# Optimization experiments

Hardware: AMD Instinct MI355X
Metric: run time of the kernel (lower is better)

The kernel has to match this reference:

```python
import jax, jax.numpy as jnp
import numpy as np

DIM = 1024
EXPANSION = 4
NUM_EXPERTS = 8
N_TOKENS = 4096
CAPACITY_FACTOR = 1.0  # also becomes the gate's k -> top-1 (bug-faithful)
EPS = 1e-6


def setup_inputs() -> dict:
    key = jax.random.key(0)
    ks = jax.random.split(key, 7)
    h = DIM * EXPANSION
    s = 0.02
    return {
        "x": jax.random.normal(ks[0], (N_TOKENS, DIM), dtype=jnp.float32),
        "w_gate": jax.random.normal(ks[1], (DIM, NUM_EXPERTS), dtype=jnp.float32) * s,
        "b_gate": jnp.zeros((NUM_EXPERTS,), dtype=jnp.float32),
        "w1": jax.random.normal(ks[2], (NUM_EXPERTS, DIM, h), dtype=jnp.float32) * s,
        "b1": jnp.zeros((NUM_EXPERTS, h), dtype=jnp.float32),
        "w2": jax.random.normal(ks[3], (NUM_EXPERTS, h, DIM), dtype=jnp.float32) * s,
        "b2": jnp.zeros((NUM_EXPERTS, DIM), dtype=jnp.float32),
    }


def fast_gelu(x):
    return x * jax.nn.sigmoid(1.702 * x)


def switch_gate(x, w_gate, b_gate):
    # x: [n, d] -> gate_scores: [n, e]
    gate_scores = jax.nn.softmax(x @ w_gate + b_gate, axis=-1)
    capacity = int(CAPACITY_FACTOR * x.shape[0])
    k = int(CAPACITY_FACTOR)  # SwitchMoE passes capacity_factor as k -> top-1
    _, top_k_idx = jax.lax.top_k(gate_scores, k)  # [n, k]
    mask = jnp.zeros_like(gate_scores).at[
        jnp.arange(x.shape[0])[:, None], top_k_idx
    ].set(1.0)
    masked = gate_scores * mask
    denom = masked.sum(axis=0, keepdims=True) + EPS  # [1, e]
    gate_scores = masked / denom * capacity
    # aux loss (use_aux_loss=True in SwitchMoE)
    load = gate_scores.sum(axis=0)               # [e]
    importance = gate_scores.sum(axis=1).mean()  # scalar
    loss = jnp.mean((load - importance) ** 2)
    return gate_scores, loss


def reference(x, w_gate, b_gate, w1, b1, w2, b2):
    gate_scores, loss = switch_gate(x, w_gate, b_gate)  # [n, e], scalar
    # dense compute-all-experts (faithful to the naive module)
    h = fast_gelu(jnp.einsum("nd,edh->enh", x, w1) + b1[:, None, :])  # [e, n, h]
    expert_out = jnp.einsum("enh,ehd->end", h, w2) + b2[:, None, :]   # [e, n, d]
    # weighted combine: sum_e gate[n,e] * expert_out[e,n,d]
    moe_output = jnp.einsum("ne,end->nd", gate_scores, expert_out)
    return moe_output, loss
```

## Files before the change

kernel.cpp:

```cpp
#include <hip/hip_runtime.h>
#include <hip/hip_bf16.h>
#include <math.h>

#define DIMK   1024
#define HDIM   4096
#define NEXP   8
#define NTOK   4096
#define EPSV   1e-6f

typedef __attribute__((ext_vector_type(4))) float  f32x4;
typedef __attribute__((ext_vector_type(8))) __bf16 bf16x8;
typedef __attribute__((ext_vector_type(4))) __bf16 bf16x4;
typedef __attribute__((ext_vector_type(2))) __bf16 bf16x2;

__device__ __forceinline__ __bf16 f2bf(float f) { return (__bf16)f; }

__global__ void init_kernel(int* counts, int* cursors, float* S) {
    int t = threadIdx.x;
    if (t < NEXP) { counts[t] = 0; cursors[t] = 0; S[t] = 0.0f; }
}

__global__ __launch_bounds__(256) void gate_kernel(
    const float* __restrict__ x, const float* __restrict__ wg,
    const float* __restrict__ bg,
    float* S, int* counts, float* score_top, int* texp)
{
    int n = blockIdx.x;
    int t = threadIdx.x;
    f32x4 xv = *(const f32x4*)(x + (size_t)n * DIMK + t * 4);

    float p[NEXP];
#pragma unroll
    for (int e = 0; e < NEXP; e++) p[e] = 0.0f;
#pragma unroll
    for (int j = 0; j < 4; j++) {
        int d = t * 4 + j;
        f32x4 wa = *(const f32x4*)(wg + (size_t)d * NEXP);
        f32x4 wb = *(const f32x4*)(wg + (size_t)d * NEXP + 4);
#pragma unroll
        for (int e = 0; e < 4; e++) { p[e] += xv[j] * wa[e]; p[e + 4] += xv[j] * wb[e]; }
    }
#pragma unroll
    for (int e = 0; e < NEXP; e++) {
#pragma unroll
        for (int off = 32; off > 0; off >>= 1)
            p[e] += __shfl_down(p[e], off, 64);
    }
    __shared__ float red[4][NEXP];
    int lane = t & 63, wv = t >> 6;
    if (lane == 0) {
#pragma unroll
        for (int e = 0; e < NEXP; e++) red[wv][e] = p[e];
    }
    __syncthreads();
    if (t == 0) {
        float l[NEXP]; float m = -1e30f;
#pragma unroll
        for (int e = 0; e < NEXP; e++) {
            l[e] = red[0][e] + red[1][e] + red[2][e] + red[3][e] + bg[e];
            m = fmaxf(m, l[e]);
        }
        float pe[NEXP]; float s = 0.0f;
#pragma unroll
        for (int e = 0; e < NEXP; e++) { pe[e] = __expf(l[e] - m); s += pe[e]; }
        int best = 0; float bv = pe[0];
#pragma unroll
        for (int e = 1; e < NEXP; e++) if (pe[e] > bv) { bv = pe[e]; best = e; }
        float sc = bv / s;
        score_top[n] = sc;
        texp[n] = best;
        atomicAdd(&S[best], sc);
        atomicAdd(&counts[best], 1);
    }
}

__global__ void finalize_kernel(const float* S, const int* counts,
                                int* offsets, float* loss_out)
{
    if (threadIdx.x == 0 && blockIdx.x == 0) {
        int off = 0;
        float loadv[NEXP]; float tot = 0.0f;
        for (int e = 0; e < NEXP; e++) { offsets[e] = off; off += counts[e]; }
        for (int e = 0; e < NEXP; e++) {
            loadv[e] = S[e] / (S[e] + EPSV) * (float)NTOK;
            tot += loadv[e];
        }
        float imp = tot / (float)NTOK;
        float loss = 0.0f;
        for (int e = 0; e < NEXP; e++) { float d = loadv[e] - imp; loss += d * d; }
        loss_out[0] = loss / (float)NEXP;
    }
}

__global__ __launch_bounds__(256) void assign_kernel(
    const int* __restrict__ texp, const float* __restrict__ score_top,
    const float* __restrict__ S, const int* __restrict__ offsets,
    int* cursors, int* perm, float* gatew)
{
    int n = blockIdx.x * 256 + threadIdx.x;
    int e = texp[n];
    int pos = atomicAdd(&cursors[e], 1);
    perm[offsets[e] + pos] = n;
    gatew[n] = score_top[n] / (S[e] + EPSV) * (float)NTOK;
}

__global__ __launch_bounds__(256) void bias_init_kernel(
    const int* __restrict__ texp, const float* __restrict__ gatew,
    const float* __restrict__ b2, float* __restrict__ out)
{
    int n = blockIdx.x;
    int t = threadIdx.x;
    int e = texp[n];
    float g = gatew[n];
    f32x4 b = *(const f32x4*)(b2 + (size_t)e * DIMK + t * 4);
    f32x4 o = { b.x * g, b.y * g, b.z * g, b.w * g };
    *(f32x4*)(out + (size_t)n * DIMK + t * 4) = o;
}

__global__ __launch_bounds__(256) void gemm1_kernel(
    const float* __restrict__ x, const float* __restrict__ w1,
    const float* __restrict__ b1,
    const int* __restrict__ perm, const int* __restrict__ counts,
    const int* __restrict__ offsets, __bf16* __restrict__ hbuf)
{
    int bx  = blockIdx.x;
    int e   = bx >> 10;
    int rem = bx & 1023;
    int mt  = rem >> 5;
    int nt  = rem & 31;
    int ce  = counts[e];
    int m0  = mt * 128;
    if (m0 >= ce) return;
    int off = offsets[e];
    int n0  = nt * 128;
    const float* B = w1 + (size_t)e * DIMK * HDIM;

    __shared__ __bf16 As[128][40];
    __shared__ __bf16 Bs[128][40];

    int t = threadIdx.x;

    const float* aptr[4];
#pragma unroll
    for (int i = 0; i < 4; i++) {
        int r  = (t >> 3) + 32 * i;
        int ri = (m0 + r < ce) ? (m0 + r) : (ce - 1);
        aptr[i] = x + (size_t)perm[off + ri] * DIMK;
    }
    int ac4 = (t & 7) * 4;

    int n4 = ((t >> 3) & 31) * 4;
    int kp = t & 7;
    const float* Bb = B + n0 + n4;

    int lane = t & 63;
    int wv   = t >> 6;
    int wm   = (wv >> 1) * 64;
    int wn   = (wv & 1) * 64;
    int lr   = lane & 15;
    int lq   = lane >> 4;

    f32x4 acc[4][4];
#pragma unroll
    for (int mi = 0; mi < 4; mi++)
#pragma unroll
        for (int ni = 0; ni < 4; ni++) acc[mi][ni] = (f32x4)0.0f;

    for (int k0 = 0; k0 < DIMK; k0 += 32) {
#pragma unroll
        for (int i = 0; i < 4; i++) {
            int r = (t >> 3) + 32 * i;
            f32x4 v = *(const f32x4*)(aptr[i] + k0 + ac4);
            bf16x4 s4 = { f2bf(v.x), f2bf(v.y), f2bf(v.z), f2bf(v.w) };
            *(bf16x4*)&As[r][ac4] = s4;
        }
#pragma unroll
        for (int i = 0; i < 2; i++) {
            int p = kp + 8 * i;
            const float* p0 = Bb + (size_t)(k0 + 2 * p) * HDIM;
            f32x4 v0 = *(const f32x4*)p0;
            f32x4 v1 = *(const f32x4*)(p0 + HDIM);
#pragma unroll
            for (int j = 0; j < 4; j++) {
                bf16x2 w = { f2bf(v0[j]), f2bf(v1[j]) };
                *(bf16x2*)&Bs[n4 + j][2 * p] = w;
            }
        }
        __syncthreads();

        bf16x8 af[4], bfr[4];
#pragma unroll
        for (int i = 0; i < 4; i++) {
            af[i]  = *(const bf16x8*)&As[wm + i * 16 + lr][lq * 8];
            bfr[i] = *(const bf16x8*)&Bs[wn + i * 16 + lr][lq * 8];
        }
#pragma unroll
        for (int mi = 0; mi < 4; mi++)
#pragma unroll
            for (int ni = 0; ni < 4; ni++)
                acc[mi][ni] = __builtin_amdgcn_mfma_f32_16x16x32_bf16(
                    af[mi], bfr[ni], acc[mi][ni], 0, 0, 0);
        __syncthreads();
    }

    const float* b1e = b1 + (size_t)e * HDIM;
#pragma unroll
    for (int mi = 0; mi < 4; mi++) {
#pragma unroll
        for (int r = 0; r < 4; r++) {
            int i = m0 + wm + mi * 16 + lq * 4 + r;
            if (i < ce) {
                __bf16* hrow = hbuf + (size_t)(off + i) * HDIM;
#pragma unroll
                for (int ni = 0; ni < 4; ni++) {
                    int j = n0 + wn + ni * 16 + lr;
                    float v = acc[mi][ni][r] + b1e[j];
                    v = v / (1.0f + __expf(-1.702f * v));
                    hrow[j] = f2bf(v);
                }
            }
        }
    }
}

__global__ __launch_bounds__(256) void gemm2_kernel(
    const __bf16* __restrict__ hbuf, const float* __restrict__ w2,
    const int* __restrict__ perm, const int* __restrict__ counts,
    const int* __restrict__ offsets, const float* __restrict__ gatew,
    float* __restrict__ out)
{
    int bx  = blockIdx.x;
    int sk  = bx & 1;
    int rest = bx >> 1;
    int e   = rest >> 9;
    int rem = rest & 511;
    int mt  = rem >> 3;
    int nt  = rem & 7;
    int ce  = counts[e];
    int m0  = mt * 64;
    if (m0 >= ce) return;
    int off = offsets[e];
    int n0  = nt * 128;
    const float* B = w2 + (size_t)e * HDIM * DIMK;

    __shared__ __bf16 As[64][72];
    __shared__ __bf16 Bs[128][72];

    int t = threadIdx.x;

    const __bf16* aptr[2];
#pragma unroll
    for (int i = 0; i < 2; i++) {
        int r  = (t >> 3) + 32 * i;
        int ri = (m0 + r < ce) ? (m0 + r) : (ce - 1);
        aptr[i] = hbuf + (size_t)(off + ri) * HDIM;
    }
    int ac8 = (t & 7) * 8;

    int n4 = ((t >> 3) & 31) * 4;
    int kp = t & 7;
    const float* Bb = B + n0 + n4;

    int lane = t & 63;
    int wv   = t >> 6;
    int wm   = (wv >> 1) * 32;
    int wn   = (wv & 1) * 64;
    int lr   = lane & 15;
    int lq   = lane >> 4;

    f32x4 acc[2][4];
#pragma unroll
    for (int mi = 0; mi < 2; mi++)
#pragma unroll
        for (int ni = 0; ni < 4; ni++) acc[mi][ni] = (f32x4)0.0f;

    int kbeg = sk * (HDIM / 2);
    int kend = kbeg + HDIM / 2;
    for (int k0 = kbeg; k0 < kend; k0 += 64) {
#pragma unroll
        for (int i = 0; i < 2; i++) {
            int r = (t >> 3) + 32 * i;
            bf16x8 v = *(const bf16x8*)(aptr[i] + k0 + ac8);
            *(bf16x8*)&As[r][ac8] = v;
        }
#pragma unroll
        for (int i = 0; i < 4; i++) {
            int p = kp + 8 * i;
            const float* p0 = Bb + (size_t)(k0 + 2 * p) * DIMK;
            f32x4 v0 = *(const f32x4*)p0;
            f32x4 v1 = *(const f32x4*)(p0 + DIMK);
#pragma unroll
            for (int j = 0; j < 4; j++) {
                bf16x2 w = { f2bf(v0[j]), f2bf(v1[j]) };
                *(bf16x2*)&Bs[n4 + j][2 * p] = w;
            }
        }
        __syncthreads();

#pragma unroll
        for (int ks = 0; ks < 2; ks++) {
            bf16x8 af[2], bfr[4];
#pragma unroll
            for (int i = 0; i < 2; i++)
                af[i] = *(const bf16x8*)&As[wm + i * 16 + lr][lq * 8 + ks * 32];
#pragma unroll
            for (int i = 0; i < 4; i++)
                bfr[i] = *(const bf16x8*)&Bs[wn + i * 16 + lr][lq * 8 + ks * 32];
#pragma unroll
            for (int mi = 0; mi < 2; mi++)
#pragma unroll
                for (int ni = 0; ni < 4; ni++)
                    acc[mi][ni] = __builtin_amdgcn_mfma_f32_16x16x32_bf16(
                        af[mi], bfr[ni], acc[mi][ni], 0, 0, 0);
        }
        __syncthreads();
    }

#pragma unroll
    for (int mi = 0; mi < 2; mi++) {
#pragma unroll
        for (int r = 0; r < 4; r++) {
            int i = m0 + wm + mi * 16 + lq * 4 + r;
            if (i < ce) {
                int tok = perm[off + i];
                float g = gatew[tok];
                float* orow = out + (size_t)tok * DIMK;
#pragma unroll
                for (int ni = 0; ni < 4; ni++) {
                    int j = n0 + wn + ni * 16 + lr;
                    atomicAdd(&orow[j], acc[mi][ni][r] * g);
                }
            }
        }
    }
}

extern "C" void kernel_launch(void* const* d_in, const int* in_sizes, int n_in,
                              void* d_out, int out_size, void* d_ws, size_t ws_size,
                              hipStream_t stream)
{
    const float* x  = (const float*)d_in[0];
    const float* wg = (const float*)d_in[1];
    const float* bg = (const float*)d_in[2];
    const float* w1 = (const float*)d_in[3];
    const float* b1 = (const float*)d_in[4];
    const float* w2 = (const float*)d_in[5];
    const float* b2 = (const float*)d_in[6];
    float* out = (float*)d_out;

    char* wsb = (char*)d_ws;
    int*   counts  = (int*)  (wsb + 0);
    int*   cursors = (int*)  (wsb + 32);
    int*   offsets = (int*)  (wsb + 64);
    float* S       = (float*)(wsb + 96);
    float* score   = (float*)(wsb + 128);
    int*   texp    = (int*)  (wsb + 16512);
    int*   perm    = (int*)  (wsb + 32896);
    float* gatew   = (float*)(wsb + 49280);
    __bf16* hbuf   = (__bf16*)(wsb + 131072);

    init_kernel<<<1, 64, 0, stream>>>(counts, cursors, S);
    gate_kernel<<<NTOK, 256, 0, stream>>>(x, wg, bg, S, counts, score, texp);
    finalize_kernel<<<1, 64, 0, stream>>>(S, counts, offsets, out + (size_t)NTOK * DIMK);
    assign_kernel<<<NTOK / 256, 256, 0, stream>>>(texp, score, S, offsets,
                                                  cursors, perm, gatew);
    bias_init_kernel<<<NTOK, 256, 0, stream>>>(texp, gatew, b2, out);
    gemm1_kernel<<<NEXP * 32 * 32, 256, 0, stream>>>(x, w1, b1, perm, counts,
                                                     offsets, hbuf);
    gemm2_kernel<<<NEXP * 64 * 8 * 2, 256, 0, stream>>>(hbuf, w2, perm, counts,
                                                        offsets, gatew, out);
}
```

Baseline: 603.5 us.

## Pre-convert weights to transposed bf16 and stream GEMM tiles via direct-to-LDS loads

Adds pre-pass kernels that convert x to bf16 and transpose/convert w1 and w2 into K-contiguous bf16 layouts every call. Both grouped GEMMs then load tiles with global_load_lds into XOR-swizzled shared memory, avoiding per-tile fp32 loads and conversions. gemm2 grows to 128x128 tiles. The transposes add a full extra read and write of both weight tensors (about 256MB read, 128MB written) per call, which may outweigh the savings since the GEMMs only touch per-expert tiles.

```diff
diff --git a/kernel.cpp b/kernel.cpp
--- a/kernel.cpp
+++ b/kernel.cpp
@@ -11,9 +11,14 @@
 typedef __attribute__((ext_vector_type(4))) float  f32x4;
 typedef __attribute__((ext_vector_type(8))) __bf16 bf16x8;
 typedef __attribute__((ext_vector_type(4))) __bf16 bf16x4;
-typedef __attribute__((ext_vector_type(2))) __bf16 bf16x2;
 
 __device__ __forceinline__ __bf16 f2bf(float f) { return (__bf16)f; }
+
+__device__ __forceinline__ void gload_lds16(const void* g, void* l) {
+    __builtin_amdgcn_global_load_lds(
+        (const __attribute__((address_space(1))) void*)g,
+        (__attribute__((address_space(3))) void*)l, 16, 0, 0);
+}
 
 __global__ void init_kernel(int* counts, int* cursors, float* S) {
     int t = threadIdx.x;
@@ -117,8 +122,50 @@
     *(f32x4*)(out + (size_t)n * DIMK + t * 4) = o;
 }
 
+__global__ __launch_bounds__(256) void cvt_kernel(
+    const float* __restrict__ x, __bf16* __restrict__ xb)
+{
+    size_t i = ((size_t)blockIdx.x * 256 + threadIdx.x) * 8;
+    f32x4 a = *(const f32x4*)(x + i);
+    f32x4 b = *(const f32x4*)(x + i + 4);
+    bf16x8 w = { f2bf(a.x), f2bf(a.y), f2bf(a.z), f2bf(a.w),
+                 f2bf(b.x), f2bf(b.y), f2bf(b.z), f2bf(b.w) };
+    *(bf16x8*)(xb + i) = w;
+}
+
+__global__ __launch_bounds__(256) void transpose_kernel(
+    const float* __restrict__ src, __bf16* __restrict__ dst, int K, int N)
+{
+    int tilesN = N >> 6;
+    int per = (K >> 6) * tilesN;
+    int e = blockIdx.x / per; int r = blockIdx.x % per;
+    int tk = r / tilesN, tn = r % tilesN;
+    const float* S = src + (size_t)e * K * N + (size_t)(tk << 6) * N + (tn << 6);
+    __bf16* D = dst + (size_t)e * K * N + (size_t)(tn << 6) * K + (tk << 6);
+    __shared__ __bf16 T[64 * 68];
+    int t = threadIdx.x;
+#pragma unroll
+    for (int i = 0; i < 4; i++) {
+        int ch = t + 256 * i;
+        int k = ch >> 4, n4 = (ch & 15) << 2;
+        f32x4 v = *(const f32x4*)(S + (size_t)k * N + n4);
+#pragma unroll
+        for (int j = 0; j < 4; j++) T[(n4 + j) * 68 + k] = f2bf(v[j]);
+    }
+    __syncthreads();
+#pragma unroll
+    for (int i = 0; i < 2; i++) {
+        int o = t + 256 * i;
+        int n = o >> 3, kc = o & 7;
+        bf16x4 a = *(const bf16x4*)&T[n * 68 + kc * 8];
+        bf16x4 b = *(const bf16x4*)&T[n * 68 + kc * 8 + 4];
+        bf16x8 w = { a.x, a.y, a.z, a.w, b.x, b.y, b.z, b.w };
+        *(bf16x8*)(D + (size_t)n * K + kc * 8) = w;
+    }
+}
+
 __global__ __launch_bounds__(256) void gemm1_kernel(
-    const float* __restrict__ x, const float* __restrict__ w1,
+    const __bf16* __restrict__ xbf, const __bf16* __restrict__ w1t,
     const float* __restrict__ b1,
     const int* __restrict__ perm, const int* __restrict__ counts,
     const int* __restrict__ offsets, __bf16* __restrict__ hbuf)
@@ -126,39 +173,35 @@
     int bx  = blockIdx.x;
     int e   = bx >> 10;
     int rem = bx & 1023;
-    int mt  = rem >> 5;
-    int nt  = rem & 31;
+    int mt  = rem >> 5, nt = rem & 31;
     int ce  = counts[e];
     int m0  = mt * 128;
     if (m0 >= ce) return;
     int off = offsets[e];
     int n0  = nt * 128;
-    const float* B = w1 + (size_t)e * DIMK * HDIM;
-
-    __shared__ __bf16 As[128][40];
-    __shared__ __bf16 Bs[128][40];
-
-    int t = threadIdx.x;
-
-    const float* aptr[4];
-#pragma unroll
-    for (int i = 0; i < 4; i++) {
-        int r  = (t >> 3) + 32 * i;
-        int ri = (m0 + r < ce) ? (m0 + r) : (ce - 1);
-        aptr[i] = x + (size_t)perm[off + ri] * DIMK;
-    }
-    int ac4 = (t & 7) * 4;
-
-    int n4 = ((t >> 3) & 31) * 4;
-    int kp = t & 7;
-    const float* Bb = B + n0 + n4;
-
-    int lane = t & 63;
-    int wv   = t >> 6;
-    int wm   = (wv >> 1) * 64;
-    int wn   = (wv & 1) * 64;
-    int lr   = lane & 15;
-    int lq   = lane >> 4;
+    const __bf16* Bsrc = w1t + (size_t)e * DIMK * HDIM + (size_t)n0 * DIMK;
+
+    __shared__ __bf16 As[128 * 64];
+    __shared__ __bf16 Bs[128 * 64];
+
+    int t = threadIdx.x;
+    int lane = t & 63, wv = t >> 6;
+    int wm = (wv >> 1) * 64, wn = (wv & 1) * 64;
+    int lr = lane & 15, lq = lane >> 4;
+
+    const __bf16* ag[4]; const __bf16* bg[4];
+    __bf16 *al[4], *bl[4];
+#pragma unroll
+    for (int c = 0; c < 4; c++) {
+        int s = c * 256 + t;
+        int row = s >> 3, pc = s & 7;
+        int gc = pc ^ (row & 7);
+        int ri = m0 + row; if (ri >= ce) ri = ce - 1;
+        ag[c] = xbf + (size_t)perm[off + ri] * DIMK + gc * 8;
+        bg[c] = Bsrc + (size_t)row * DIMK + gc * 8;
+        al[c] = As + s * 8;
+        bl[c] = Bs + s * 8;
+    }
 
     f32x4 acc[4][4];
 #pragma unroll
@@ -166,55 +209,46 @@
 #pragma unroll
         for (int ni = 0; ni < 4; ni++) acc[mi][ni] = (f32x4)0.0f;
 
-    for (int k0 = 0; k0 < DIMK; k0 += 32) {
-#pragma unroll
-        for (int i = 0; i < 4; i++) {
-            int r = (t >> 3) + 32 * i;
-            f32x4 v = *(const f32x4*)(aptr[i] + k0 + ac4);
-            bf16x4 s4 = { f2bf(v.x), f2bf(v.y), f2bf(v.z), f2bf(v.w) };
-            *(bf16x4*)&As[r][ac4] = s4;
-        }
-#pragma unroll
-        for (int i = 0; i < 2; i++) {
-            int p = kp + 8 * i;
-            const float* p0 = Bb + (size_t)(k0 + 2 * p) * HDIM;
-            f32x4 v0 = *(const f32x4*)p0;
-            f32x4 v1 = *(const f32x4*)(p0 + HDIM);
-#pragma unroll
-            for (int j = 0; j < 4; j++) {
-                bf16x2 w = { f2bf(v0[j]), f2bf(v1[j]) };
-                *(bf16x2*)&Bs[n4 + j][2 * p] = w;
+    for (int k0 = 0; k0 < DIMK; k0 += 64) {
+#pragma unroll
+        for (int c = 0; c < 4; c++) gload_lds16(ag[c], al[c]);
+#pragma unroll
+        for (int c = 0; c < 4; c++) gload_lds16(bg[c], bl[c]);
+        __syncthreads();
+#pragma unroll
+        for (int ks = 0; ks < 2; ks++) {
+            bf16x8 af[4], bfr[4];
+#pragma unroll
+            for (int i = 0; i < 4; i++) {
+                int ra = wm + i * 16 + lr;
+                af[i]  = *(const bf16x8*)(As + ra * 64 + (((ks * 4 + lq) ^ (ra & 7)) << 3));
+                int rb = wn + i * 16 + lr;
+                bfr[i] = *(const bf16x8*)(Bs + rb * 64 + (((ks * 4 + lq) ^ (rb & 7)) << 3));
             }
+#pragma unroll
+            for (int mi = 0; mi < 4; mi++)
+#pragma unroll
+                for (int ni = 0; ni < 4; ni++)
+                    acc[mi][ni] = __builtin_amdgcn_mfma_f32_16x16x32_bf16(
+                        af[mi], bfr[ni], acc[mi][ni], 0, 0, 0);
         }
         __syncthreads();
-
-        bf16x8 af[4], bfr[4];
-#pragma unroll
-        for (int i = 0; i < 4; i++) {
-            af[i]  = *(const bf16x8*)&As[wm + i * 16 + lr][lq * 8];
-            bfr[i] = *(const bf16x8*)&Bs[wn + i * 16 + lr][lq * 8];
-        }
-#pragma unroll
-        for (int mi = 0; mi < 4; mi++)
-#pragma unroll
-            for (int ni = 0; ni < 4; ni++)
-                acc[mi][ni] = __builtin_amdgcn_mfma_f32_16x16x32_bf16(
-                    af[mi], bfr[ni], acc[mi][ni], 0, 0, 0);
-        __syncthreads();
+#pragma unroll
+        for (int c = 0; c < 4; c++) { ag[c] += 64; bg[c] += 64; }
     }
 
     const float* b1e = b1 + (size_t)e * HDIM;
 #pragma unroll
     for (int mi = 0; mi < 4; mi++) {
 #pragma unroll
-        for (int r = 0; r < 4; r++) {
-            int i = m0 + wm + mi * 16 + lq * 4 + r;
+        for (int rr = 0; rr < 4; rr++) {
+            int i = m0 + wm + mi * 16 + lq * 4 + rr;
             if (i < ce) {
                 __bf16* hrow = hbuf + (size_t)(off + i) * HDIM;
 #pragma unroll
                 for (int ni = 0; ni < 4; ni++) {
                     int j = n0 + wn + ni * 16 + lr;
-                    float v = acc[mi][ni][r] + b1e[j];
+                    float v = acc[mi][ni][rr] + b1e[j];
                     v = v / (1.0f + __expf(-1.702f * v));
                     hrow[j] = f2bf(v);
                 }
@@ -224,103 +258,84 @@
 }
 
 __global__ __launch_bounds__(256) void gemm2_kernel(
-    const __bf16* __restrict__ hbuf, const float* __restrict__ w2,
+    const __bf16* __restrict__ hbuf, const __bf16* __restrict__ w2t,
     const int* __restrict__ perm, const int* __restrict__ counts,
     const int* __restrict__ offsets, const float* __restrict__ gatew,
     float* __restrict__ out)
 {
-    int bx  = blockIdx.x;
-    int sk  = bx & 1;
-    int rest = bx >> 1;
-    int e   = rest >> 9;
-    int rem = rest & 511;
-    int mt  = rem >> 3;
-    int nt  = rem & 7;
-    int ce  = counts[e];
-    int m0  = mt * 64;
+    int bx = blockIdx.x;
+    int sk = bx & 1; int r = bx >> 1;
+    int e = r >> 8; int rem = r & 255;
+    int mt = rem >> 3, nt = rem & 7;
+    int ce = counts[e];
+    int m0 = mt * 128;
     if (m0 >= ce) return;
     int off = offsets[e];
-    int n0  = nt * 128;
-    const float* B = w2 + (size_t)e * HDIM * DIMK;
-
-    __shared__ __bf16 As[64][72];
-    __shared__ __bf16 Bs[128][72];
-
-    int t = threadIdx.x;
-
-    const __bf16* aptr[2];
-#pragma unroll
-    for (int i = 0; i < 2; i++) {
-        int r  = (t >> 3) + 32 * i;
-        int ri = (m0 + r < ce) ? (m0 + r) : (ce - 1);
-        aptr[i] = hbuf + (size_t)(off + ri) * HDIM;
-    }
-    int ac8 = (t & 7) * 8;
-
-    int n4 = ((t >> 3) & 31) * 4;
-    int kp = t & 7;
-    const float* Bb = B + n0 + n4;
-
-    int lane = t & 63;
-    int wv   = t >> 6;
-    int wm   = (wv >> 1) * 32;
-    int wn   = (wv & 1) * 64;
-    int lr   = lane & 15;
-    int lq   = lane >> 4;
-
-    f32x4 acc[2][4];
-#pragma unroll
-    for (int mi = 0; mi < 2; mi++)
+    int n0 = nt * 128;
+    int kbeg = sk * (HDIM / 2);
+    const __bf16* Bsrc = w2t + (size_t)e * HDIM * DIMK + (size_t)n0 * HDIM;
+
+    __shared__ __bf16 As[128 * 64];
+    __shared__ __bf16 Bs[128 * 64];
+
+    int t = threadIdx.x;
+    int lane = t & 63, wv = t >> 6;
+    int wm = (wv >> 1) * 64, wn = (wv & 1) * 64;
+    int lr = lane & 15, lq = lane >> 4;
+
+    const __bf16* ag[4]; const __bf16* bg[4];
+    __bf16 *al[4], *bl[4];
+#pragma unroll
+    for (int c = 0; c < 4; c++) {
+        int s = c * 256 + t;
+        int row = s >> 3, pc = s & 7;
+        int gc = pc ^ (row & 7);
+        int ri = m0 + row; if (ri >= ce) ri = ce - 1;
+        ag[c] = hbuf + (size_t)(off + ri) * HDIM + kbeg + gc * 8;
+        bg[c] = Bsrc + (size_t)row * HDIM + kbeg + gc * 8;
+        al[c] = As + s * 8;
+        bl[c] = Bs + s * 8;
+    }
+
+    f32x4 acc[4][4];
+#pragma unroll
+    for (int mi = 0; mi < 4; mi++)
 #pragma unroll
         for (int ni = 0; ni < 4; ni++) acc[mi][ni] = (f32x4)0.0f;
 
-    int kbeg = sk * (HDIM / 2);
-    int kend = kbeg + HDIM / 2;
-    for (int k0 = kbeg; k0 < kend; k0 += 64) {
-#pragma unroll
-        for (int i = 0; i < 2; i++) {
-            int r = (t >> 3) + 32 * i;
-            bf16x8 v = *(const bf16x8*)(aptr[i] + k0 + ac8);
-            *(bf16x8*)&As[r][ac8] = v;
-        }
-#pragma unroll
-        for (int i = 0; i < 4; i++) {
-            int p = kp + 8 * i;
-            const float* p0 = Bb + (size_t)(k0 + 2 * p) * DIMK;
-            f32x4 v0 = *(const f32x4*)p0;
-            f32x4 v1 = *(const f32x4*)(p0 + DIMK);
-#pragma unroll
-            for (int j = 0; j < 4; j++) {
-                bf16x2 w = { f2bf(v0[j]), f2bf(v1[j]) };
-                *(bf16x2*)&Bs[n4 + j][2 * p] = w;
+    for (int k0 = 0; k0 < HDIM / 2; k0 += 64) {
+#pragma unroll
+        for (int c = 0; c < 4; c++) gload_lds16(ag[c], al[c]);
+#pragma unroll
+        for (int c = 0; c < 4; c++) gload_lds16(bg[c], bl[c]);
+        __syncthreads();
+#pragma unroll
+        for (int ks = 0; ks < 2; ks++) {
+            bf16x8 af[4], bfr[4];
+#pragma unroll
+            for (int i = 0; i < 4; i++) {
+                int ra = wm + i * 16 + lr;
+                af[i]  = *(const bf16x8*)(As + ra * 64 + (((ks * 4 + lq) ^ (ra & 7)) << 3));
+                int rb = wn + i * 16 + lr;
+                bfr[i] = *(const bf16x8*)(Bs + rb * 64 + (((ks * 4 + lq) ^ (rb & 7)) << 3));
             }
-        }
-        __syncthreads();
-
-#pragma unroll
-        for (int ks = 0; ks < 2; ks++) {
-            bf16x8 af[2], bfr[4];
-#pragma unroll
-            for (int i = 0; i < 2; i++)
-                af[i] = *(const bf16x8*)&As[wm + i * 16 + lr][lq * 8 + ks * 32];
-#pragma unroll
-            for (int i = 0; i < 4; i++)
-                bfr[i] = *(const bf16x8*)&Bs[wn + i * 16 + lr][lq * 8 + ks * 32];
-#pragma unroll
-            for (int mi = 0; mi < 2; mi++)
+#pragma unroll
+            for (int mi = 0; mi < 4; mi++)
 #pragma unroll
                 for (int ni = 0; ni < 4; ni++)
                     acc[mi][ni] = __builtin_amdgcn_mfma_f32_16x16x32_bf16(
                         af[mi], bfr[ni], acc[mi][ni], 0, 0, 0);
         }
         __syncthreads();
-    }
-
-#pragma unroll
-    for (int mi = 0; mi < 2; mi++) {
-#pragma unroll
-        for (int r = 0; r < 4; r++) {
-            int i = m0 + wm + mi * 16 + lq * 4 + r;
+#pragma unroll
+        for (int c = 0; c < 4; c++) { ag[c] += 64; bg[c] += 64; }
+    }
+
+#pragma unroll
+    for (int mi = 0; mi < 4; mi++) {
+#pragma unroll
+        for (int rr = 0; rr < 4; rr++) {
+            int i = m0 + wm + mi * 16 + lq * 4 + rr;
             if (i < ce) {
                 int tok = perm[off + i];
                 float g = gatew[tok];
@@ -328,7 +343,7 @@
 #pragma unroll
                 for (int ni = 0; ni < 4; ni++) {
                     int j = n0 + wn + ni * 16 + lr;
-                    atomicAdd(&orow[j], acc[mi][ni][r] * g);
+                    atomicAdd(&orow[j], acc[mi][ni][rr] * g);
                 }
             }
         }
@@ -358,6 +373,9 @@
     int*   perm    = (int*)  (wsb + 32896);
     float* gatew   = (float*)(wsb + 49280);
     __bf16* hbuf   = (__bf16*)(wsb + 131072);
+    __bf16* xbf    = (__bf16*)(wsb + 33685504);
+    __bf16* w1t    = (__bf16*)(wsb + 42074112);
+    __bf16* w2t    = (__bf16*)(wsb + 109182976);
 
     init_kernel<<<1, 64, 0, stream>>>(counts, cursors, S);
     gate_kernel<<<NTOK, 256, 0, stream>>>(x, wg, bg, S, counts, score, texp);
@@ -365,8 +383,11 @@
     assign_kernel<<<NTOK / 256, 256, 0, stream>>>(texp, score, S, offsets,
                                                   cursors, perm, gatew);
     bias_init_kernel<<<NTOK, 256, 0, stream>>>(texp, gatew, b2, out);
-    gemm1_kernel<<<NEXP * 32 * 32, 256, 0, stream>>>(x, w1, b1, perm, counts,
+    cvt_kernel<<<(NTOK * DIMK) / (256 * 8), 256, 0, stream>>>(x, xbf);
+    transpose_kernel<<<NEXP * 16 * 64, 256, 0, stream>>>(w1, w1t, DIMK, HDIM);
+    transpose_kernel<<<NEXP * 64 * 16, 256, 0, stream>>>(w2, w2t, HDIM, DIMK);
+    gemm1_kernel<<<NEXP * 32 * 32, 256, 0, stream>>>(xbf, w1t, b1, perm, counts,
                                                      offsets, hbuf);
-    gemm2_kernel<<<NEXP * 64 * 8 * 2, 256, 0, stream>>>(hbuf, w2, perm, counts,
+    gemm2_kernel<<<NEXP * 32 * 8 * 2, 256, 0, stream>>>(hbuf, w2t, perm, counts,
                                                         offsets, gatew, out);
 }
```

Measured after the change: 578.8 us. -4.1%, faster.
